# Optimization experiments

Hardware: AMD Instinct MI355X
Metric: run time of the kernel (lower is better)

The kernel has to match this reference:

```python
import jax, jax.numpy as jnp
import numpy as np

ROPE_THETA = 10000.0

def _apply_rope(x, theta=ROPE_THETA):
    # x: [B, H, L, d_head]
    L, d_k = x.shape[-2], x.shape[-1]
    inv_freq = 1.0 / (theta ** (jnp.arange(0, d_k, 2, dtype=jnp.float32) / d_k))  # [d_k/2]
    ang = jnp.arange(L, dtype=jnp.float32)[:, None] * inv_freq[None, :]           # [L, d_k/2]
    ang = jnp.repeat(ang, 2, axis=-1)                                             # [L, d_k] interleaved
    xr = x.reshape(x.shape[:-1] + (d_k // 2, 2))
    rot = jnp.stack((-xr[..., 1], xr[..., 0]), axis=-1).reshape(x.shape)
    return x * jnp.cos(ang) + rot * jnp.sin(ang)

def setup_inputs() -> dict:
    key = jax.random.key(0)
    k1, k2, k3 = jax.random.split(key, 3)
    B, L, D = 2, 2048, 2048
    std_qkv = np.sqrt(2.0 / (D + 3 * D)).astype(np.float32)
    std_o = np.sqrt(2.0 / (D + D)).astype(np.float32)
    return {
        "x": jax.random.normal(k1, (B, L, D), dtype=jnp.float32),
        "W_qkv": jax.random.normal(k2, (3 * D, D), dtype=jnp.float32) * std_qkv,
        "W_o": jax.random.normal(k3, (D, D), dtype=jnp.float32) * std_o,
    }

def reference(x, W_qkv, W_o):
    B, L, D = x.shape
    H = 16
    dh = D // H
    qkv = jnp.einsum('bld,ed->ble', x, W_qkv)            # [B, L, 3D]
    q, k, v = jnp.split(qkv, 3, axis=-1)
    # [B, H, L, dh]
    q = q.reshape(B, L, H, dh).transpose(0, 2, 1, 3)
    k = k.reshape(B, L, H, dh).transpose(0, 2, 1, 3)
    v = v.reshape(B, L, H, dh).transpose(0, 2, 1, 3)
    q = _apply_rope(q)
    k = _apply_rope(k)
    scale = 1.0 / np.sqrt(dh).astype(np.float32)
    att = jnp.einsum('bhqd,bhkd->bhqk', q, k) * scale    # [B, H, L, L]
    causal = jnp.tril(jnp.ones((L, L), dtype=bool))
    att = jnp.where(causal, att, -jnp.inf)
    p = jax.nn.softmax(att, axis=-1)
    y = jnp.einsum('bhqk,bhkd->bhqd', p, v)              # [B, H, L, dh]
    y = y.transpose(0, 2, 1, 3).reshape(B, L, D)
    return jnp.einsum('bld,ed->ble', y, W_o)
```

## Files before the change

kernel.cpp:

```cpp
#include <hip/hip_runtime.h>
#include <math.h>

typedef __bf16 bf16x8 __attribute__((ext_vector_type(8)));
typedef float f32x4 __attribute__((ext_vector_type(4)));
typedef unsigned short us8 __attribute__((ext_vector_type(8)));

#define B_ 2
#define L_ 2048
#define D_ 2048
#define H_ 16
#define DH 128

__device__ __forceinline__ unsigned short f2b(float f) {
  union { float f; unsigned u; } v; v.f = f;
  unsigned u = v.u;
  return (unsigned short)((u + 0x7fffu + ((u >> 16) & 1u)) >> 16);
}
__device__ __forceinline__ float b2f(unsigned short h) {
  union { unsigned u; float f; } v; v.u = ((unsigned)h) << 16;
  return v.f;
}

#define GLD16(g, l) __builtin_amdgcn_global_load_lds(                          \
    (const __attribute__((address_space(1))) void*)(g),                        \
    (__attribute__((address_space(3))) void*)(l), 16, 0, 0)

#define SBAR() __builtin_amdgcn_s_barrier()
#define LGK0() asm volatile("s_waitcnt lgkmcnt(0)")
#define SCB0() __builtin_amdgcn_sched_barrier(0)
#define VMC3() asm volatile("s_waitcnt vmcnt(3)" ::: "memory")
#define VMC0() asm volatile("s_waitcnt vmcnt(0)" ::: "memory")

__device__ __forceinline__ unsigned ldsoff(const void* p) {
  return (unsigned)(unsigned long long)(const __attribute__((address_space(3))) char*)p;
}
__device__ __forceinline__ bf16x8 dsr128(unsigned a) {
  bf16x8 r;
  asm volatile("ds_read_b128 %0, %1" : "=v"(r) : "v"(a));
  return r;
}

__global__ void f32_to_bf16_3(const float* __restrict__ a, int na4,
                              const float* __restrict__ b, int nb4,
                              const float* __restrict__ c, int nc4,
                              unsigned short* __restrict__ oa,
                              unsigned short* __restrict__ ob,
                              unsigned short* __restrict__ oc) {
  const int total = na4 + nb4 + nc4;
  int i = blockIdx.x * blockDim.x + threadIdx.x;
  const int stride = gridDim.x * blockDim.x;
  for (; i < total; i += stride) {
    const float* src;
    unsigned short* dst;
    int j = i;
    if (j < na4) { src = a; dst = oa; }
    else if (j < na4 + nb4) { j -= na4; src = b; dst = ob; }
    else { j -= na4 + nb4; src = c; dst = oc; }
    const float4 v = ((const float4*)src)[j];
    ushort4 o;
    o.x = f2b(v.x); o.y = f2b(v.y); o.z = f2b(v.z); o.w = f2b(v.w);
    ((ushort4*)dst)[j] = o;
  }
}

__global__ __launch_bounds__(512, 4)
void gemm_qkv(const unsigned short* __restrict__ A,
              const unsigned short* __restrict__ Bm,
              unsigned short* __restrict__ Qb,
              unsigned short* __restrict__ Kb,
              unsigned short* __restrict__ Vf, int M, int K) {
  __shared__ __align__(16) unsigned short lA[3][128 * 32];
  __shared__ __align__(16) unsigned short lB[3][256 * 32];
  const int tid = threadIdx.x;
  const int w = tid >> 6, lane = tid & 63;
  const int lo = lane & 15, hi = lane >> 4;
  const int mh = w >> 2;
  const int wn = (w & 3) * 64;
  const int GM = M >> 7;
  const int nwg = gridDim.x;
  const int f = blockIdx.x;
  const int v = (f & 7) * (nwg >> 3) + (f >> 3);
  const int bn = v / GM, bm = v % GM;
  const int NT = K >> 5;

  const int srow = tid >> 2;
  const int gs = (tid & 3) ^ ((srow >> 1) & 3);
  auto stA = [&](int buf, int tile) {
    GLD16(A + (long)(bm * 128 + srow) * K + tile * 32 + gs * 8,
          &lA[buf][(tid & ~63) * 8]);
  };
  auto stB = [&](int buf, int u, int tile) {
    GLD16(Bm + (long)(bn * 256 + u * 128 + srow) * K + tile * 32 + gs * 8,
          &lB[buf][u * 4096 + (tid & ~63) * 8]);
  };

  unsigned aoff[4], boff[4];
#pragma unroll
  for (int mi = 0; mi < 4; ++mi) {
    const int r = mh * 64 + mi * 16 + lo;
    aoff[mi] = ldsoff(&lA[0][0]) + r * 64 + ((hi ^ ((r >> 1) & 3)) * 16);
  }
#pragma unroll
  for (int ni = 0; ni < 4; ++ni) {
    const int rb = wn + ni * 16 + lo;
    boff[ni] = ldsoff(&lB[0][0]) + rb * 64 + ((hi ^ ((rb >> 1) & 3)) * 16);
  }

  f32x4 acc[4][4] = {};

  stA(0, 0); stB(0, 0, 0); stB(0, 1, 0);
  stA(1, 1); stB(1, 0, 1); stB(1, 1, 1);
  VMC3();
  SBAR();

  for (int t = 0; t < NT; ++t) {
    const int bt = t % 3;
    const int b2 = (t + 2) % 3;
    const bool nx = (t + 2 < NT);
    const unsigned ab = (unsigned)(bt * 8192);
    const unsigned bb = (unsigned)(bt * 16384);
    bf16x8 af[4], bfv[4];
#pragma unroll
    for (int mi = 0; mi < 4; ++mi) af[mi] = dsr128(aoff[mi] + ab);
#pragma unroll
    for (int ni = 0; ni < 4; ++ni) bfv[ni] = dsr128(boff[ni] + bb);
    if (nx) { stA(b2, t + 2); stB(b2, 0, t + 2); stB(b2, 1, t + 2); }
    LGK0(); SCB0();
    __builtin_amdgcn_s_setprio(1);
#pragma unroll
    for (int mi = 0; mi < 4; ++mi)
#pragma unroll
      for (int ni = 0; ni < 4; ++ni)
        acc[mi][ni] = __builtin_amdgcn_mfma_f32_16x16x32_bf16(
            af[mi], bfv[ni], acc[mi][ni], 0, 0, 0);
    __builtin_amdgcn_s_setprio(0);
    if (t < NT - 2) VMC3(); else VMC0();
    SBAR();
  }

  const int r0 = bm * 128 + mh * 64;
  const int h = (bn & 7) * 2 + (wn >> 7);
  const int d0 = wn & 64;
  if (bn < 16) {
    unsigned short* dst = (bn < 8) ? Qb : Kb;
    const float sc = (bn < 8) ? 0.12751743f : 1.0f;
#pragma unroll
    for (int ni = 0; ni < 4; ++ni) {
      const int d = d0 + ni * 16 + lo;
      const float invr = exp2f(-(float)(d >> 1) * 0.20762050593045077f) *
                         0.15915494309189535f;
#pragma unroll
      for (int mi = 0; mi < 4; ++mi) {
#pragma unroll
        for (int r = 0; r < 4; ++r) {
          const int row = r0 + mi * 16 + hi * 4 + r;
          const int b = row >> 11, l = row & (L_ - 1);
          const float rev = __builtin_amdgcn_fractf((float)l * invr);
          const float sn = __builtin_amdgcn_sinf(rev);
          const float cs = __builtin_amdgcn_cosf(rev);
          const float v0 = acc[mi][ni][r] * sc;
          const float vp = __shfl_xor(v0, 1);
          const float ov = (d & 1) ? (v0 * cs + vp * sn)
                                   : (v0 * cs - vp * sn);
          dst[((long)(b * H_ + h) * L_ + l) * DH + d] = f2b(ov);
        }
      }
    }
  } else {
#pragma unroll
    for (int ni = 0; ni < 4; ++ni) {
      const int d = d0 + ni * 16 + lo;
#pragma unroll
      for (int mi = 0; mi < 4; ++mi) {
        const int row0 = r0 + mi * 16 + hi * 4;
        const int b = row0 >> 11, l0 = row0 & (L_ - 1);
        const size_t base =
            (((size_t)(b * H_ + h) * 64 + (l0 >> 5)) * 8 + (d >> 4)) * 512;
        const int fl = (d & 15) + ((l0 >> 3) & 3) * 16;
        ushort4 pk;
        pk.x = f2b(acc[mi][ni][0]);
        pk.y = f2b(acc[mi][ni][1]);
        pk.z = f2b(acc[mi][ni][2]);
        pk.w = f2b(acc[mi][ni][3]);
        *(ushort4*)&Vf[base + fl * 8 + (l0 & 7)] = pk;
      }
    }
  }
}

template <bool OUT_BF16>
__global__ __launch_bounds__(512, 4)
void gemmk32(const unsigned short* __restrict__ A,
             const unsigned short* __restrict__ Bm,
             void* __restrict__ Cv, int M, int N, int K) {
  __shared__ __align__(16) unsigned short lA[3][128 * 32];
  __shared__ __align__(16) unsigned short lB[3][256 * 32];
  const int tid = threadIdx.x;
  const int w = tid >> 6, lane = tid & 63;
  const int lo = lane & 15, hi = lane >> 4;
  const int mh = w >> 2;
  const int wn = (w & 3) * 64;
  const int GM = M >> 7;
  const int nwg = gridDim.x;
  const int f = blockIdx.x;
  const int v = (f & 7) * (nwg >> 3) + (f >> 3);
  const int bn = v / GM, bm = v % GM;
  const int NT = K >> 5;

  const int srow = tid >> 2;
  const int gs = (tid & 3) ^ ((srow >> 1) & 3);
  auto stA = [&](int buf, int tile) {
    GLD16(A + (long)(bm * 128 + srow) * K + tile * 32 + gs * 8,
          &lA[buf][(tid & ~63) * 8]);
  };
  auto stB = [&](int buf, int u, int tile) {
    GLD16(Bm + (long)(bn * 256 + u * 128 + srow) * K + tile * 32 + gs * 8,
          &lB[buf][u * 4096 + (tid & ~63) * 8]);
  };

  unsigned aoff[4], boff[4];
#pragma unroll
  for (int mi = 0; mi < 4; ++mi) {
    const int r = mh * 64 + mi * 16 + lo;
    aoff[mi] = ldsoff(&lA[0][0]) + r * 64 + ((hi ^ ((r >> 1) & 3)) * 16);
  }
#pragma unroll
  for (int ni = 0; ni < 4; ++ni) {
    const int rb = wn + ni * 16 + lo;
    boff[ni] = ldsoff(&lB[0][0]) + rb * 64 + ((hi ^ ((rb >> 1) & 3)) * 16);
  }

  f32x4 acc[4][4] = {};

  stA(0, 0); stB(0, 0, 0); stB(0, 1, 0);
  stA(1, 1); stB(1, 0, 1); stB(1, 1, 1);
  VMC3();
  SBAR();

  for (int t = 0; t < NT; ++t) {
    const int bt = t % 3;
    const int b2 = (t + 2) % 3;
    const bool nx = (t + 2 < NT);
    const unsigned ab = (unsigned)(bt * 8192);
    const unsigned bb = (unsigned)(bt * 16384);
    bf16x8 af[4], bfv[4];
#pragma unroll
    for (int mi = 0; mi < 4; ++mi) af[mi] = dsr128(aoff[mi] + ab);
#pragma unroll
    for (int ni = 0; ni < 4; ++ni) bfv[ni] = dsr128(boff[ni] + bb);
    if (nx) { stA(b2, t + 2); stB(b2, 0, t + 2); stB(b2, 1, t + 2); }
    LGK0(); SCB0();
    __builtin_amdgcn_s_setprio(1);
#pragma unroll
    for (int mi = 0; mi < 4; ++mi)
#pragma unroll
      for (int ni = 0; ni < 4; ++ni)
        acc[mi][ni] = __builtin_amdgcn_mfma_f32_16x16x32_bf16(
            af[mi], bfv[ni], acc[mi][ni], 0, 0, 0);
    __builtin_amdgcn_s_setprio(0);
    if (t < NT - 2) VMC3(); else VMC0();
    SBAR();
  }

  const int r0 = bm * 128 + mh * 64;
  const int c0 = bn * 256 + wn;
#pragma unroll
  for (int mi = 0; mi < 4; ++mi) {
#pragma unroll
    for (int r = 0; r < 4; ++r) {
      const long row = r0 + mi * 16 + hi * 4 + r;
#pragma unroll
      for (int ni = 0; ni < 4; ++ni) {
        const int col = c0 + ni * 16 + lo;
        if (OUT_BF16)
          ((unsigned short*)Cv)[row * N + col] = f2b(acc[mi][ni][r]);
        else
          ((float*)Cv)[row * N + col] = acc[mi][ni][r];
      }
    }
  }
}

__global__ __launch_bounds__(256, 2)
void flash_attn3(const unsigned short* __restrict__ Q,
                 const unsigned short* __restrict__ Kg,
                 const unsigned short* __restrict__ Vf,
                 unsigned short* __restrict__ Y) {
  const int p = blockIdx.x;
  const int tA = p, tB = (L_ / 64 - 1) - p;
  const int h = blockIdx.y, b = blockIdx.z;
  const int tid = threadIdx.x;
  const int wave = tid >> 6, lane = tid & 63;
  const int lo = lane & 15, hi = lane >> 4;
  const int swz = (lo & 7) << 4;
  const int qA = tA * 64 + wave * 16;
  const int qB = tB * 64 + wave * 16;
  const long hoff = ((long)(b * H_ + h)) * L_ * DH;
  const unsigned short* Qh = Q + hoff;
  const unsigned short* Kh = Kg + hoff;
  const unsigned short* Vfh = Vf + ((size_t)(b * H_ + h)) * (64 * 8 * 512);

  __shared__ unsigned short lK[2][64 * 128];
  __shared__ unsigned short pl[4][2][16 * 72];
  unsigned short* plA = &pl[wave][0][0];
  unsigned short* plB = &pl[wave][1][0];

  auto stage = [&](int bufi, int kv0s) {
    unsigned short* bk = &lK[bufi][0];
#pragma unroll
    for (int j = 0; j < 4; ++j) {
      const int c = j * 256 + tid;
      const int row = c >> 4;
      const int soff = ((c & 15) ^ (row & 7)) << 3;
      GLD16(Kh + (long)(kv0s + row) * DH + soff, &bk[(c & ~63) * 8]);
    }
  };

  bf16x8 qfA[4], qfB[4];
#pragma unroll
  for (int s = 0; s < 4; ++s) {
    qfA[s] = *(const bf16x8*)&Qh[(long)(qA + lo) * DH + s * 32 + hi * 8];
    qfB[s] = *(const bf16x8*)&Qh[(long)(qB + lo) * DH + s * 32 + hi * 8];
  }

  float mA = -INFINITY, lsA = 0.f, mB = -INFINITY, lsB = 0.f;
  f32x4 yA[8] = {}, yB[8] = {};

  auto softmax = [&](f32x4 (&st)[4], float& m, float& lsum, f32x4 (&yacc)[8],
                     unsigned short* plw, int qw, int kv0) {
    if (kv0 + 63 > qw) {
      const int d0 = qw + lo - kv0 - hi * 4;
#pragma unroll
      for (int t = 0; t < 4; ++t) {
        const int dt = d0 - t * 16;
#pragma unroll
        for (int r = 0; r < 4; ++r)
          if (r > dt) st[t][r] = -INFINITY;
      }
    }
    float tm0 = fmaxf(fmaxf(st[0][0], st[0][1]), fmaxf(st[0][2], st[0][3]));
    float tm1 = fmaxf(fmaxf(st[1][0], st[1][1]), fmaxf(st[1][2], st[1][3]));
    float tm2 = fmaxf(fmaxf(st[2][0], st[2][1]), fmaxf(st[2][2], st[2][3]));
    float tm3 = fmaxf(fmaxf(st[3][0], st[3][1]), fmaxf(st[3][2], st[3][3]));
    float rm = fmaxf(fmaxf(tm0, tm1), fmaxf(tm2, tm3));
    rm = fmaxf(rm, __shfl_xor(rm, 16));
    rm = fmaxf(rm, __shfl_xor(rm, 32));
    if (!__all(rm <= m + 8.f)) {
      const float mn = fmaxf(m, rm);
      const float alpha = exp2f(m - mn);
      m = mn;
      lsum *= alpha;
      float ar[4];
#pragma unroll
      for (int r = 0; r < 4; ++r) ar[r] = __shfl(alpha, hi * 4 + r);
#pragma unroll
      for (int t2 = 0; t2 < 8; ++t2)
#pragma unroll
        for (int r = 0; r < 4; ++r) yacc[t2][r] *= ar[r];
    }
    float rs = 0.f;
#pragma unroll
    for (int t = 0; t < 4; ++t) {
#pragma unroll
      for (int r2 = 0; r2 < 2; ++r2) {
        const float e0 = exp2f(st[t][2 * r2] - m);
        const float e1 = exp2f(st[t][2 * r2 + 1] - m);
        rs += e0 + e1;
        const unsigned short u0 = __builtin_bit_cast(unsigned short, (__bf16)e0);
        const unsigned short u1 = __builtin_bit_cast(unsigned short, (__bf16)e1);
        *(unsigned*)&plw[lo * 72 + t * 16 + hi * 4 + 2 * r2] =
            (unsigned)u0 | ((unsigned)u1 << 16);
      }
    }
    rs += __shfl_xor(rs, 16);
    rs += __shfl_xor(rs, 32);
    lsum += rs;
  };

  const int nIter = tB + 1;
  stage(0, 0);
  __syncthreads();

  for (int it = 0; it < nIter; ++it) {
    const int kv0 = it * 64;
    const bool aAct = (it <= tA);
    if (it + 1 < nIter) stage((it + 1) & 1, kv0 + 64);
    const char* bkc = (const char*)&lK[it & 1][0];
    f32x4 stA[4] = {}, stB[4] = {};
    if (aAct) {
#pragma unroll
      for (int s = 0; s < 4; ++s) {
        const int inner = (lo * 256 + s * 64 + hi * 16) ^ swz;
#pragma unroll
        for (int t = 0; t < 4; ++t) {
          const bf16x8 kf = *(const bf16x8*)(bkc + t * 4096 + inner);
          stA[t] = __builtin_amdgcn_mfma_f32_16x16x32_bf16(kf, qfA[s], stA[t], 0, 0, 0);
          stB[t] = __builtin_amdgcn_mfma_f32_16x16x32_bf16(kf, qfB[s], stB[t], 0, 0, 0);
        }
      }
    } else {
#pragma unroll
      for (int s = 0; s < 4; ++s) {
        const int inner = (lo * 256 + s * 64 + hi * 16) ^ swz;
#pragma unroll
        for (int t = 0; t < 4; ++t) {
          const bf16x8 kf = *(const bf16x8*)(bkc + t * 4096 + inner);
          stB[t] = __builtin_amdgcn_mfma_f32_16x16x32_bf16(kf, qfB[s], stB[t], 0, 0, 0);
        }
      }
    }
    const unsigned short* vbase = Vfh + (size_t)(it * 16) * 512 + lane * 8;
    bf16x8 vf[16];
#pragma unroll
    for (int t2 = 0; t2 < 16; ++t2)
      vf[t2] = *(const bf16x8*)(vbase + (size_t)t2 * 512);
    if (aAct) softmax(stA, mA, lsA, yA, plA, qA, kv0);
    softmax(stB, mB, lsB, yB, plB, qB, kv0);
#pragma unroll
    for (int kt = 0; kt < 2; ++kt) {
      const bf16x8 pfB = *(const bf16x8*)&plB[lo * 72 + kt * 32 + hi * 8];
#pragma unroll
      for (int t2 = 0; t2 < 8; ++t2)
        yB[t2] = __builtin_amdgcn_mfma_f32_16x16x32_bf16(pfB, vf[kt * 8 + t2], yB[t2], 0, 0, 0);
      if (aAct) {
        const bf16x8 pfA = *(const bf16x8*)&plA[lo * 72 + kt * 32 + hi * 8];
#pragma unroll
        for (int t2 = 0; t2 < 8; ++t2)
          yA[t2] = __builtin_amdgcn_mfma_f32_16x16x32_bf16(pfA, vf[kt * 8 + t2], yA[t2], 0, 0, 0);
      }
    }
    __syncthreads();
  }

  auto wout = [&](f32x4 (&yacc)[8], float lsum, int qw) {
    const float inv = 1.f / lsum;
    float ir[4];
#pragma unroll
    for (int r = 0; r < 4; ++r) ir[r] = __shfl(inv, hi * 4 + r);
#pragma unroll
    for (int r = 0; r < 4; ++r) {
      const long row = qw + hi * 4 + r;
      unsigned short* yrow = Y + ((long)b * L_ + row) * D_ + h * DH;
#pragma unroll
      for (int t2 = 0; t2 < 8; ++t2)
        yrow[t2 * 16 + lo] = f2b(yacc[t2][r] * ir[r]);
    }
  };
  wout(yA, lsA, qA);
  wout(yB, lsB, qB);
}

extern "C" void kernel_launch(void* const* d_in, const int* in_sizes, int n_in,
                              void* d_out, int out_size, void* d_ws, size_t ws_size,
                              hipStream_t stream) {
  const float* x = (const float*)d_in[0];
  const float* wqkv = (const float*)d_in[1];
  const float* wo = (const float*)d_in[2];
  float* out = (float*)d_out;

  unsigned short* ws = (unsigned short*)d_ws;
  const size_t N_X = (size_t)B_ * L_ * D_;
  const size_t N_WQKV = (size_t)3 * D_ * D_;
  const size_t N_WO = (size_t)D_ * D_;
  const size_t N_HEAD = (size_t)B_ * H_ * L_ * DH;
  unsigned short* xb = ws;
  unsigned short* wqkb = xb + N_X;
  unsigned short* wob = wqkb + N_WQKV;
  unsigned short* Qb = wob + N_WO;
  unsigned short* Kb = Qb + N_HEAD;
  unsigned short* Vf = Kb + N_HEAD;
  unsigned short* Yb = Vf + N_HEAD;
  const size_t need = (size_t)(Yb + N_HEAD - ws) * sizeof(unsigned short);
  if (ws_size < need) return;

  f32_to_bf16_3<<<2048, 256, 0, stream>>>(
      x, (int)(N_X / 4), wqkv, (int)(N_WQKV / 4), wo, (int)(N_WO / 4),
      xb, wqkb, wob);

  gemm_qkv<<<(B_ * L_ / 128) * (3 * D_ / 256), 512, 0, stream>>>(
      xb, wqkb, Qb, Kb, Vf, B_ * L_, D_);

  flash_attn3<<<dim3(16, H_, B_), 256, 0, stream>>>(Qb, Kb, Vf, Yb);

  gemmk32<false><<<(B_ * L_ / 128) * (D_ / 256), 512, 0, stream>>>(
      Yb, wob, out, B_ * L_, D_, D_);
}
```

Before: 259.8 us.

## Rewrite QKV GEMM as 256x256 tile with ping-pong interleaved MFMA/load schedule

Replaces the 128x256 triple-buffered QKV GEMM with a 256x256 tile kernel that uses K-tiles of 64, split into half-tile LDS buffers that are double buffered. Loads of the next half-tiles are interleaved with four MFMA quadrants per stage, with barriers between them. The goal is more reuse per LDS byte and better overlap of global loads with MFMA work. The cost is higher register pressure (a 32-accumulator tile), more LDS, fewer workgroups and many barriers. It also adds s_setprio around the MFMA blocks in flash attention.

Result: slower. 272.4 us (+4.8%).

```diff
diff --git a/kernel.cpp b/kernel.cpp
--- a/kernel.cpp
+++ b/kernel.cpp
@@ -28,6 +28,7 @@
 #define SBAR() __builtin_amdgcn_s_barrier()
 #define LGK0() asm volatile("s_waitcnt lgkmcnt(0)")
 #define SCB0() __builtin_amdgcn_sched_barrier(0)
+#define VMC4() asm volatile("s_waitcnt vmcnt(4)" ::: "memory")
 #define VMC3() asm volatile("s_waitcnt vmcnt(3)" ::: "memory")
 #define VMC0() asm volatile("s_waitcnt vmcnt(0)" ::: "memory")
 
@@ -63,84 +64,113 @@
   }
 }
 
-__global__ __launch_bounds__(512, 4)
-void gemm_qkv(const unsigned short* __restrict__ A,
-              const unsigned short* __restrict__ Bm,
-              unsigned short* __restrict__ Qb,
-              unsigned short* __restrict__ Kb,
-              unsigned short* __restrict__ Vf, int M, int K) {
-  __shared__ __align__(16) unsigned short lA[3][128 * 32];
-  __shared__ __align__(16) unsigned short lB[3][256 * 32];
+#define LOAD_A8(BUF, MH)                                                       \
+  _Pragma("unroll") for (int q = 0; q < 4; ++q) {                              \
+    const int rh = (MH) * 64 + q * 16 + lo;                                    \
+    _Pragma("unroll") for (int s = 0; s < 2; ++s)                              \
+        af[q][s] = *(const bf16x8*)&lA[BUF][wm]                                \
+            [rh * 64 + (((s * 4 + hi) ^ (rh & 7)) * 8)];                       \
+  }
+
+#define LOAD_B8(BUF, NH)                                                       \
+  _Pragma("unroll") for (int j = 0; j < 2; ++j) {                              \
+    const int rb = blb + (NH) * 32 + j * 16 + lo;                              \
+    _Pragma("unroll") for (int s = 0; s < 2; ++s)                              \
+        bfr[NH][j][s] = *(const bf16x8*)&lB[BUF][hb]                           \
+            [rb * 64 + (((s * 4 + hi) ^ (rb & 7)) * 8)];                       \
+  }
+
+#define MFMA16(MH, NH)                                                         \
+  do {                                                                         \
+    __builtin_amdgcn_s_setprio(1);                                             \
+    _Pragma("unroll") for (int q = 0; q < 4; ++q)                              \
+        _Pragma("unroll") for (int j = 0; j < 2; ++j)                          \
+            _Pragma("unroll") for (int s = 0; s < 2; ++s)                      \
+                acc[(MH) * 4 + q][(NH) * 2 + j] =                              \
+                    __builtin_amdgcn_mfma_f32_16x16x32_bf16(                   \
+                        af[q][s], bfr[NH][j][s],                               \
+                        acc[(MH) * 4 + q][(NH) * 2 + j], 0, 0, 0);             \
+    __builtin_amdgcn_s_setprio(0);                                             \
+  } while (0)
+
+__global__ __launch_bounds__(512)
+void gemm_qkv8(const unsigned short* __restrict__ A,
+               const unsigned short* __restrict__ Bm,
+               unsigned short* __restrict__ Qb,
+               unsigned short* __restrict__ Kb,
+               unsigned short* __restrict__ Vf, int M, int K) {
+  __shared__ __align__(16) unsigned short lA[2][2][128 * 64];
+  __shared__ __align__(16) unsigned short lB[2][2][128 * 64];
   const int tid = threadIdx.x;
   const int w = tid >> 6, lane = tid & 63;
   const int lo = lane & 15, hi = lane >> 4;
-  const int mh = w >> 2;
-  const int wn = (w & 3) * 64;
-  const int GM = M >> 7;
-  const int nwg = gridDim.x;
+  const int wm = w >> 2;
+  const int wn4 = w & 3;
+  const int hb = wn4 >> 1;
+  const int blb = (wn4 & 1) * 64;
+  const int GM = M >> 8;
   const int f = blockIdx.x;
-  const int v = (f & 7) * (nwg >> 3) + (f >> 3);
+  const int v = (f & 7) * (gridDim.x >> 3) + (f >> 3);
   const int bn = v / GM, bm = v % GM;
-  const int NT = K >> 5;
-
-  const int srow = tid >> 2;
-  const int gs = (tid & 3) ^ ((srow >> 1) & 3);
-  auto stA = [&](int buf, int tile) {
-    GLD16(A + (long)(bm * 128 + srow) * K + tile * 32 + gs * 8,
-          &lA[buf][(tid & ~63) * 8]);
-  };
-  auto stB = [&](int buf, int u, int tile) {
-    GLD16(Bm + (long)(bn * 256 + u * 128 + srow) * K + tile * 32 + gs * 8,
-          &lB[buf][u * 4096 + (tid & ~63) * 8]);
-  };
-
-  unsigned aoff[4], boff[4];
-#pragma unroll
-  for (int mi = 0; mi < 4; ++mi) {
-    const int r = mh * 64 + mi * 16 + lo;
-    aoff[mi] = ldsoff(&lA[0][0]) + r * 64 + ((hi ^ ((r >> 1) & 3)) * 16);
-  }
-#pragma unroll
-  for (int ni = 0; ni < 4; ++ni) {
-    const int rb = wn + ni * 16 + lo;
-    boff[ni] = ldsoff(&lB[0][0]) + rb * 64 + ((hi ^ ((rb >> 1) & 3)) * 16);
-  }
-
-  f32x4 acc[4][4] = {};
-
-  stA(0, 0); stB(0, 0, 0); stB(0, 1, 0);
-  stA(1, 1); stB(1, 0, 1); stB(1, 1, 1);
-  VMC3();
+  const int NI = K >> 7;
+
+  const int row64 = tid >> 3;
+  const int gs = (tid & 7) ^ (row64 & 7);
+  auto stA = [&](int buf, int h, int tile) {
+#pragma unroll
+    for (int u = 0; u < 2; ++u)
+      GLD16(A + (long)(bm * 256 + h * 128 + u * 64 + row64) * K + tile * 64 + gs * 8,
+            &lA[buf][h][u * 4096 + (tid & ~63) * 8]);
+  };
+  auto stB = [&](int buf, int h, int tile) {
+#pragma unroll
+    for (int u = 0; u < 2; ++u)
+      GLD16(Bm + (long)(bn * 256 + h * 128 + u * 64 + row64) * K + tile * 64 + gs * 8,
+            &lB[buf][h][u * 4096 + (tid & ~63) * 8]);
+  };
+
+  f32x4 acc[8][4] = {};
+  bf16x8 af[4][2], bfr[2][2][2];
+
+  stB(0, 0, 0); stB(0, 1, 0); stA(0, 0, 0); stA(0, 1, 0);
+  stB(1, 0, 1); stB(1, 1, 1);
+  VMC4();
   SBAR();
 
-  for (int t = 0; t < NT; ++t) {
-    const int bt = t % 3;
-    const int b2 = (t + 2) % 3;
-    const bool nx = (t + 2 < NT);
-    const unsigned ab = (unsigned)(bt * 8192);
-    const unsigned bb = (unsigned)(bt * 16384);
-    bf16x8 af[4], bfv[4];
-#pragma unroll
-    for (int mi = 0; mi < 4; ++mi) af[mi] = dsr128(aoff[mi] + ab);
-#pragma unroll
-    for (int ni = 0; ni < 4; ++ni) bfv[ni] = dsr128(boff[ni] + bb);
-    if (nx) { stA(b2, t + 2); stB(b2, 0, t + 2); stB(b2, 1, t + 2); }
-    LGK0(); SCB0();
-    __builtin_amdgcn_s_setprio(1);
-#pragma unroll
-    for (int mi = 0; mi < 4; ++mi)
-#pragma unroll
-      for (int ni = 0; ni < 4; ++ni)
-        acc[mi][ni] = __builtin_amdgcn_mfma_f32_16x16x32_bf16(
-            af[mi], bfv[ni], acc[mi][ni], 0, 0, 0);
-    __builtin_amdgcn_s_setprio(0);
-    if (t < NT - 2) VMC3(); else VMC0();
+  for (int i = 0; i < NI; ++i) {
+    const int tOdd = 2 * i + 1;
+    const bool nx = (i + 1 < NI);
+    LOAD_A8(0, 0) LOAD_B8(0, 0)
+    stA(1, 0, tOdd);
+    SBAR(); LGK0(); MFMA16(0, 0); SBAR();
+    LOAD_B8(0, 1)
+    stA(1, 1, tOdd);
+    SBAR(); LGK0(); MFMA16(0, 1); SBAR();
+    LOAD_A8(0, 1)
+    if (nx) stB(0, 0, tOdd + 1);
+    SBAR(); LGK0(); MFMA16(1, 1); SBAR();
+    if (nx) stB(0, 1, tOdd + 1);
+    SBAR(); MFMA16(1, 0);
+    if (nx) VMC4(); else VMC0();
     SBAR();
-  }
-
-  const int r0 = bm * 128 + mh * 64;
-  const int h = (bn & 7) * 2 + (wn >> 7);
-  const int d0 = wn & 64;
+    LOAD_A8(1, 0) LOAD_B8(1, 0)
+    if (nx) stA(0, 0, tOdd + 1);
+    SBAR(); LGK0(); MFMA16(0, 0); SBAR();
+    LOAD_B8(1, 1)
+    if (nx) stA(0, 1, tOdd + 1);
+    SBAR(); LGK0(); MFMA16(0, 1); SBAR();
+    LOAD_A8(1, 1)
+    if (nx) stB(1, 0, tOdd + 2);
+    SBAR(); LGK0(); MFMA16(1, 1); SBAR();
+    if (nx) stB(1, 1, tOdd + 2);
+    SBAR(); MFMA16(1, 0);
+    if (nx) VMC4();
+    SBAR();
+  }
+
+  const int r0 = bm * 256 + wm * 128;
+  const int h = (bn & 7) * 2 + (wn4 >> 1);
+  const int d0 = (wn4 & 1) * 64;
   if (bn < 16) {
     unsigned short* dst = (bn < 8) ? Qb : Kb;
     const float sc = (bn < 8) ? 0.12751743f : 1.0f;
@@ -150,7 +180,7 @@
       const float invr = exp2f(-(float)(d >> 1) * 0.20762050593045077f) *
                          0.15915494309189535f;
 #pragma unroll
-      for (int mi = 0; mi < 4; ++mi) {
+      for (int mi = 0; mi < 8; ++mi) {
 #pragma unroll
         for (int r = 0; r < 4; ++r) {
           const int row = r0 + mi * 16 + hi * 4 + r;
@@ -171,7 +201,7 @@
     for (int ni = 0; ni < 4; ++ni) {
       const int d = d0 + ni * 16 + lo;
 #pragma unroll
-      for (int mi = 0; mi < 4; ++mi) {
+      for (int mi = 0; mi < 8; ++mi) {
         const int row0 = r0 + mi * 16 + hi * 4;
         const int b = row0 >> 11, l0 = row0 & (L_ - 1);
         const size_t base =
@@ -388,6 +418,7 @@
     const char* bkc = (const char*)&lK[it & 1][0];
     f32x4 stA[4] = {}, stB[4] = {};
     if (aAct) {
+      __builtin_amdgcn_s_setprio(1);
 #pragma unroll
       for (int s = 0; s < 4; ++s) {
         const int inner = (lo * 256 + s * 64 + hi * 16) ^ swz;
@@ -398,7 +429,9 @@
           stB[t] = __builtin_amdgcn_mfma_f32_16x16x32_bf16(kf, qfB[s], stB[t], 0, 0, 0);
         }
       }
+      __builtin_amdgcn_s_setprio(0);
     } else {
+      __builtin_amdgcn_s_setprio(1);
 #pragma unroll
       for (int s = 0; s < 4; ++s) {
         const int inner = (lo * 256 + s * 64 + hi * 16) ^ swz;
@@ -408,6 +441,7 @@
           stB[t] = __builtin_amdgcn_mfma_f32_16x16x32_bf16(kf, qfB[s], stB[t], 0, 0, 0);
         }
       }
+      __builtin_amdgcn_s_setprio(0);
     }
     const unsigned short* vbase = Vfh + (size_t)(it * 16) * 512 + lane * 8;
     bf16x8 vf[16];
@@ -416,6 +450,7 @@
       vf[t2] = *(const bf16x8*)(vbase + (size_t)t2 * 512);
     if (aAct) softmax(stA, mA, lsA, yA, plA, qA, kv0);
     softmax(stB, mB, lsB, yB, plB, qB, kv0);
+    __builtin_amdgcn_s_setprio(1);
 #pragma unroll
     for (int kt = 0; kt < 2; ++kt) {
       const bf16x8 pfB = *(const bf16x8*)&plB[lo * 72 + kt * 32 + hi * 8];
@@ -429,6 +464,7 @@
           yA[t2] = __builtin_amdgcn_mfma_f32_16x16x32_bf16(pfA, vf[kt * 8 + t2], yA[t2], 0, 0, 0);
       }
     }
+    __builtin_amdgcn_s_setprio(0);
     __syncthreads();
   }
 
@@ -477,7 +513,7 @@
       x, (int)(N_X / 4), wqkv, (int)(N_WQKV / 4), wo, (int)(N_WO / 4),
       xb, wqkb, wob);
 
-  gemm_qkv<<<(B_ * L_ / 128) * (3 * D_ / 256), 512, 0, stream>>>(
+  gemm_qkv8<<<(B_ * L_ / 256) * (3 * D_ / 256), 512, 0, stream>>>(
       xb, wqkb, Qb, Kb, Vf, B_ * L_, D_);
 
   flash_attn3<<<dim3(16, H_, B_), 256, 0, stream>>>(Qb, Kb, Vf, Yb);
```
